# Kernel optimization log

Hardware: AMD Instinct MI355X
Metric: run time of the kernel (lower is better)

Reference implementation:

```python
import jax, jax.numpy as jnp
import numpy as np

B, C, L = 8, 512, 2048
HEADS, DIM_HEAD = 8, 64
HID = HEADS * DIM_HEAD  # 512


def setup_inputs() -> dict:
    key = jax.random.key(0)
    k1, k2, k3, k4 = jax.random.split(key, 4)
    x = jax.random.normal(k1, (B, C, L), dtype=jnp.float32)
    # Conv1d kernel_size=1 weights stored as [out, in] matrices
    w_qkv = jax.random.normal(k2, (3 * HID, C), dtype=jnp.float32) * (1.0 / np.sqrt(C))
    w_out = jax.random.normal(k3, (C, HID), dtype=jnp.float32) * (1.0 / np.sqrt(HID))
    b_out = jax.random.normal(k4, (C,), dtype=jnp.float32) * 0.01
    return {"x": x, "w_qkv": w_qkv, "w_out": w_out, "b_out": b_out}


def reference(x, w_qkv, w_out, b_out):
    scale = DIM_HEAD ** (-0.5)
    # 1x1 conv == channel-wise linear: [b,c,l] -> [b,3*hid,l]
    qkv = jnp.einsum('oc,bcl->bol', w_qkv, x)
    q, k, v = jnp.split(qkv, 3, axis=1)
    # split heads: b (h d) l -> b h d l
    split = lambda t: t.reshape(x.shape[0], HEADS, DIM_HEAD, t.shape[-1])
    q, k, v = split(q) * scale, split(k), split(v)
    sim = jnp.einsum('bhdi,bhdj->bhij', q, k)  # [b,h,l,l]
    attn = jax.nn.softmax(sim, axis=-1)
    out = jnp.einsum('bhij,bhdj->bhid', attn, v)  # [b,h,l,d]
    # b h l d -> b (h d) l
    out = jnp.transpose(out, (0, 1, 3, 2)).reshape(x.shape[0], HID, x.shape[-1])
    return jnp.einsum('oc,bcl->bol', w_out, out) + b_out[None, :, None]
```

## Files before the change

kernel.cpp:

```cpp
#include <hip/hip_runtime.h>

#define NB 8
#define NC 512
#define NL 2048
#define NH 8
#define ND 64
#define NHID 512

typedef float f32x4 __attribute__((ext_vector_type(4)));
typedef short bf16x8 __attribute__((ext_vector_type(8)));
typedef unsigned uint32x2 __attribute__((ext_vector_type(2)));
typedef unsigned uint32x4 __attribute__((ext_vector_type(4)));

__device__ __forceinline__ unsigned short f2bf(float x) {
    unsigned u = __float_as_uint(x);
    u += 0x7fffu + ((u >> 16) & 1u);
    return (unsigned short)(u >> 16);
}

__device__ __forceinline__ unsigned pack_bf16_ru(float lo, float hi) {
    unsigned a = __float_as_uint(lo) + 0x8000u;
    unsigned b = __float_as_uint(hi) + 0x8000u;
#if __has_builtin(__builtin_amdgcn_perm)
    return __builtin_amdgcn_perm(b, a, 0x07060302u);
#else
    return (a >> 16) | (b & 0xffff0000u);
#endif
}

__device__ __forceinline__ float fexp2(float x) {
#if __has_builtin(__builtin_amdgcn_exp2f)
    return __builtin_amdgcn_exp2f(x);
#else
    return exp2f(x);
#endif
}

__device__ __forceinline__ void gll16(const unsigned short* g, unsigned short* l) {
    __builtin_amdgcn_global_load_lds(
        (const __attribute__((address_space(1))) unsigned int*)g,
        (__attribute__((address_space(3))) unsigned int*)l, 16, 0, 0);
}

__device__ __forceinline__ void pfr_quad_swap(unsigned &a, unsigned &b) {
#if __has_builtin(__builtin_amdgcn_permlane32_swap) && __has_builtin(__builtin_amdgcn_permlane16_swap)
    uint32x2 r0 = __builtin_amdgcn_permlane32_swap(a, b, false, false);
    uint32x2 r1 = __builtin_amdgcn_permlane16_swap(r0[0], r0[1], false, false);
    a = r1[0];
    b = r1[1];
#else
    const int lane = (int)(threadIdx.x & 63);
    const int li = lane & 15, quad = lane >> 4;
    const int s0 = (li + ((quad & 1) << 5)) << 2;
    const int s1 = (li + 16 + ((quad & 1) << 5)) << 2;
    int ra = __builtin_amdgcn_ds_bpermute(s0, (int)a);
    int rb = __builtin_amdgcn_ds_bpermute(s0, (int)b);
    int ta = __builtin_amdgcn_ds_bpermute(s1, (int)a);
    int tb = __builtin_amdgcn_ds_bpermute(s1, (int)b);
    const bool lo = quad < 2;
    a = (unsigned)(lo ? ra : rb);
    b = (unsigned)(lo ? ta : tb);
#endif
}

__global__ __launch_bounds__(256) void xpose_kernel(
    const float* __restrict__ x, unsigned short* __restrict__ xT)
{
    __shared__ unsigned short T[64 * 65];
    const int tid = threadIdx.x;
    const int l0 = blockIdx.x * 64, c0 = blockIdx.y * 64, b = blockIdx.z;

    const int ll = tid & 63, cl0 = tid >> 6;
    #pragma unroll
    for (int i = 0; i < 16; i++) {
        const int cl = cl0 + 4 * i;
        T[cl * 65 + ll] = f2bf(x[((size_t)(b * NC + c0 + cl)) * NL + l0 + ll]);
    }
    __syncthreads();
    const int cg = tid & 7, lr = tid >> 3;
    #pragma unroll
    for (int rep = 0; rep < 2; rep++) {
        const int l = lr + rep * 32;
        unsigned u[4];
        #pragma unroll
        for (int j = 0; j < 4; j++) {
            unsigned short a = T[(cg * 8 + 2 * j) * 65 + l];
            unsigned short c = T[(cg * 8 + 2 * j + 1) * 65 + l];
            u[j] = (unsigned)a | ((unsigned)c << 16);
        }
        uint4 val; val.x = u[0]; val.y = u[1]; val.z = u[2]; val.w = u[3];
        *(uint4*)&xT[((size_t)(b * NL + l0 + l)) * NC + c0 + cg * 8] = val;
    }
}

__global__ __launch_bounds__(256) void wconv_kernel(
    const float* __restrict__ src, unsigned short* __restrict__ dst,
    int n8, int nscale8, float scale)
{
    const int idx = blockIdx.x * 256 + threadIdx.x;
    if (idx >= n8) return;
    const float s = (idx < nscale8) ? scale : 1.0f;
    float4 a = *(const float4*)&src[(size_t)idx * 8];
    float4 c = *(const float4*)&src[(size_t)idx * 8 + 4];
    uint4 val;
    val.x = (unsigned)f2bf(a.x * s) | ((unsigned)f2bf(a.y * s) << 16);
    val.y = (unsigned)f2bf(a.z * s) | ((unsigned)f2bf(a.w * s) << 16);
    val.z = (unsigned)f2bf(c.x * s) | ((unsigned)f2bf(c.y * s) << 16);
    val.w = (unsigned)f2bf(c.z * s) | ((unsigned)f2bf(c.w * s) << 16);
    *(uint4*)&dst[(size_t)idx * 8] = val;
}

__global__ __launch_bounds__(256) void qkv_proj_kernel(
    const unsigned short* __restrict__ xT, const unsigned short* __restrict__ wq,
    unsigned short* __restrict__ qb, unsigned short* __restrict__ kb,
    unsigned short* __restrict__ vb)
{
    __shared__ __align__(16) unsigned short Xt[128 * 64];
    __shared__ __align__(16) unsigned short Wt[128 * 64];
    const int tid = threadIdx.x;
    const int wave = tid >> 6, lane = tid & 63;
    const int quad = lane >> 4, li = lane & 15;
    const int o0 = blockIdx.x * 128, l0 = blockIdx.y * 128, b = blockIdx.z;

    const f32x4 fzero = {0.f, 0.f, 0.f, 0.f};
    f32x4 acc[2][8];
    #pragma unroll
    for (int mt = 0; mt < 2; mt++)
        #pragma unroll
        for (int nt = 0; nt < 8; nt++) acc[mt][nt] = fzero;

    const int srow = lane >> 3, schk = lane & 7;

    for (int c0 = 0; c0 < NC; c0 += 64) {
        #pragma unroll
        for (int i = 0; i < 4; i++) {
            const int r = wave * 32 + i * 8 + srow;
            gll16(xT + ((size_t)(b * NL + l0 + r)) * NC + c0 + ((schk ^ (r & 7)) * 8),
                  &Xt[(wave * 32 + i * 8) * 64]);
            gll16(wq + (size_t)(o0 + r) * NC + c0 + ((schk ^ (r & 7)) * 8),
                  &Wt[(wave * 32 + i * 8) * 64]);
        }
        __syncthreads();
        #pragma unroll
        for (int kc = 0; kc < 2; kc++) {
            const int sw = ((kc * 4 + quad) ^ (li & 7)) * 8;
            bf16x8 afr0 = *(const bf16x8*)&Xt[(wave * 32 + li) * 64 + sw];
            bf16x8 afr1 = *(const bf16x8*)&Xt[(wave * 32 + 16 + li) * 64 + sw];
            #pragma unroll
            for (int nt = 0; nt < 8; nt++) {
                bf16x8 bfr = *(const bf16x8*)&Wt[(nt * 16 + li) * 64 + sw];
                acc[0][nt] = __builtin_amdgcn_mfma_f32_16x16x32_bf16(afr0, bfr, acc[0][nt], 0, 0, 0);
                acc[1][nt] = __builtin_amdgcn_mfma_f32_16x16x32_bf16(afr1, bfr, acc[1][nt], 0, 0, 0);
            }
        }
        __syncthreads();
    }

    const int lr0 = l0 + wave * 32;
    if (o0 < 1024) {
        unsigned short* dst = (o0 < 512) ? qb : kb;
        #pragma unroll
        for (int mt = 0; mt < 2; mt++)
            #pragma unroll
            for (int nt = 0; nt < 8; nt++) {
                int oc = (o0 & 511) + nt * 16 + li;
                int hh = oc >> 6, d = oc & 63;
                size_t base =
                    ((size_t)((b * NH + hh) * NL) + lr0 + mt * 16 + quad * 4) * ND + d;
                #pragma unroll
                for (int r = 0; r < 4; r++)
                    dst[base + (size_t)r * ND] = f2bf(acc[mt][nt][r]);
            }
    } else {
        #pragma unroll
        for (int mt = 0; mt < 2; mt++)
            #pragma unroll
            for (int nt = 0; nt < 8; nt++) {
                int oc = (o0 - 1024) + nt * 16 + li;
                int hh = oc >> 6, d = oc & 63;
                size_t base = ((size_t)((b * NH + hh) * ND) + d) * NL +
                              lr0 + mt * 16 + quad * 4;
                uint2 pv;
                pv.x = (unsigned)f2bf(acc[mt][nt][0]) | ((unsigned)f2bf(acc[mt][nt][1]) << 16);
                pv.y = (unsigned)f2bf(acc[mt][nt][2]) | ((unsigned)f2bf(acc[mt][nt][3]) << 16);
                *(uint2*)&vb[base] = pv;
            }
    }
}

__global__ __launch_bounds__(256, 4) void attn_kernel(
    const unsigned short* __restrict__ qb, const unsigned short* __restrict__ kb,
    const unsigned short* __restrict__ vb, unsigned short* __restrict__ at)
{
    __shared__ __align__(16) unsigned short Kt[2][64 * 64];
    __shared__ __align__(16) unsigned short Vt[2][64 * 64];
    const int tid = threadIdx.x;
    const int wave = tid >> 6, lane = tid & 63;
    const int quad = lane >> 4, li = lane & 15;
    const int qt = blockIdx.x, h = blockIdx.y, b = blockIdx.z;
    const int bh = b * NH + h;
    const unsigned short* Qb = qb + (size_t)bh * NL * ND;
    const unsigned short* Kb = kb + (size_t)bh * NL * ND;
    const unsigned short* Vb = vb + (size_t)bh * ND * NL;

    bf16x8 qfr[2][2];
    #pragma unroll
    for (int mt = 0; mt < 2; mt++)
        #pragma unroll
        for (int kc = 0; kc < 2; kc++)
            qfr[mt][kc] = *(const bf16x8*)&Qb[(size_t)(qt * 128 + wave * 32 + mt * 16 + li) * ND +
                                             kc * 32 + quad * 8];

    const f32x4 fzero = {0.f, 0.f, 0.f, 0.f};
    f32x4 oacc[2][4];
    #pragma unroll
    for (int mt = 0; mt < 2; mt++)
        #pragma unroll
        for (int dt = 0; dt < 4; dt++) oacc[mt][dt] = fzero;

    f32x4 lsacc0 = fzero, lsacc1 = fzero;
    const short one_bf = (short)0x3F80;
    const bf16x8 ones = {one_bf, one_bf, one_bf, one_bf,
                         one_bf, one_bf, one_bf, one_bf};

    const int rrow = lane >> 3;
    const int rchk = lane & 7;

    auto stage = [&](int buf, int j0) {
        #pragma unroll
        for (int i = 0; i < 2; i++) {
            const int jrow = wave * 16 + i * 8 + rrow;
            gll16(Kb + (size_t)(j0 + jrow) * ND + ((rchk ^ (jrow & 7)) * 8),
                  &Kt[buf][(wave * 16 + i * 8) * 64]);
            const int drow = wave * 16 + i * 8 + rrow;
            gll16(Vb + (size_t)drow * NL + j0 + ((rchk ^ (drow & 7)) * 8),
                  &Vt[buf][(wave * 16 + i * 8) * 64]);
        }
    };

    stage(0, 0);
    __syncthreads();

    #pragma unroll 2
    for (int kt = 0; kt < 32; kt++) {
        const int cur = kt & 1;
        if (kt < 31) stage(cur ^ 1, (kt + 1) * 64);

        #pragma unroll
        for (int c = 0; c < 2; c++) {
            f32x4 st00 = fzero, st01 = fzero, st10 = fzero, st11 = fzero;
            #pragma unroll
            for (int dk = 0; dk < 2; dk++) {
                const int sw = ((dk * 4 + quad) ^ (li & 7)) * 8;
                bf16x8 kf0 = *(const bf16x8*)&Kt[cur][((2 * c + 0) * 16 + li) * 64 + sw];
                bf16x8 kf1 = *(const bf16x8*)&Kt[cur][((2 * c + 1) * 16 + li) * 64 + sw];
                st00 = __builtin_amdgcn_mfma_f32_16x16x32_bf16(kf0, qfr[0][dk], st00, 0, 0, 0);
                st01 = __builtin_amdgcn_mfma_f32_16x16x32_bf16(kf1, qfr[0][dk], st01, 0, 0, 0);
                st10 = __builtin_amdgcn_mfma_f32_16x16x32_bf16(kf0, qfr[1][dk], st10, 0, 0, 0);
                st11 = __builtin_amdgcn_mfma_f32_16x16x32_bf16(kf1, qfr[1][dk], st11, 0, 0, 0);
            }

            unsigned p000, p001, p010, p011, p100, p101, p110, p111;
            {
                float a0 = fexp2(st00[0]), a1 = fexp2(st00[1]),
                      a2 = fexp2(st00[2]), a3 = fexp2(st00[3]);
                float b0 = fexp2(st01[0]), b1 = fexp2(st01[1]),
                      b2 = fexp2(st01[2]), b3 = fexp2(st01[3]);
                p000 = pack_bf16_ru(a0, a1); p001 = pack_bf16_ru(a2, a3);
                p010 = pack_bf16_ru(b0, b1); p011 = pack_bf16_ru(b2, b3);
            }
            {
                float a0 = fexp2(st10[0]), a1 = fexp2(st10[1]),
                      a2 = fexp2(st10[2]), a3 = fexp2(st10[3]);
                float b0 = fexp2(st11[0]), b1 = fexp2(st11[1]),
                      b2 = fexp2(st11[2]), b3 = fexp2(st11[3]);
                p100 = pack_bf16_ru(a0, a1); p101 = pack_bf16_ru(a2, a3);
                p110 = pack_bf16_ru(b0, b1); p111 = pack_bf16_ru(b2, b3);
            }

            pfr_quad_swap(p000, p010);
            pfr_quad_swap(p001, p011);
            pfr_quad_swap(p100, p110);
            pfr_quad_swap(p101, p111);

            uint32x4 u0 = {p000, p001, p010, p011};
            uint32x4 u1 = {p100, p101, p110, p111};
            bf16x8 pf0 = __builtin_bit_cast(bf16x8, u0);
            bf16x8 pf1 = __builtin_bit_cast(bf16x8, u1);

            lsacc0 = __builtin_amdgcn_mfma_f32_16x16x32_bf16(ones, pf0, lsacc0, 0, 0, 0);
            lsacc1 = __builtin_amdgcn_mfma_f32_16x16x32_bf16(ones, pf1, lsacc1, 0, 0, 0);

            #pragma unroll
            for (int dt = 0; dt < 4; dt++) {
                const int swv = ((c * 4 + quad) ^ (li & 7)) * 8;
                bf16x8 vfr = *(const bf16x8*)&Vt[cur][(dt * 16 + li) * 64 + swv];
                oacc[0][dt] = __builtin_amdgcn_mfma_f32_16x16x32_bf16(vfr, pf0, oacc[0][dt], 0, 0, 0);
                oacc[1][dt] = __builtin_amdgcn_mfma_f32_16x16x32_bf16(vfr, pf1, oacc[1][dt], 0, 0, 0);
            }
        }
        __syncthreads();
    }

    #pragma unroll
    for (int mt = 0; mt < 2; mt++) {
        const float rl = 1.0f / (mt ? lsacc1[0] : lsacc0[0]);
        const int l = qt * 128 + wave * 32 + mt * 16 + li;
        #pragma unroll
        for (int dt = 0; dt < 4; dt++) {
            uint2 ov;
            ov.x = (unsigned)f2bf(oacc[mt][dt][0] * rl) |
                   ((unsigned)f2bf(oacc[mt][dt][1] * rl) << 16);
            ov.y = (unsigned)f2bf(oacc[mt][dt][2] * rl) |
                   ((unsigned)f2bf(oacc[mt][dt][3] * rl) << 16);
            *(uint2*)&at[((size_t)(b * NL + l)) * NHID + h * ND + dt * 16 + quad * 4] = ov;
        }
    }
}

__global__ __launch_bounds__(256) void out_proj_kernel(
    const unsigned short* __restrict__ at, const unsigned short* __restrict__ wo,
    const float* __restrict__ bias, float* __restrict__ out)
{
    __shared__ __align__(16) unsigned short Wt[128 * 64];
    __shared__ __align__(16) unsigned short At[128 * 64];
    const int tid = threadIdx.x;
    const int wave = tid >> 6, lane = tid & 63;
    const int quad = lane >> 4, li = lane & 15;
    const int o0 = blockIdx.x * 128, l0 = blockIdx.y * 128, b = blockIdx.z;

    const f32x4 fzero = {0.f, 0.f, 0.f, 0.f};
    f32x4 acc[2][8];
    #pragma unroll
    for (int mt = 0; mt < 2; mt++)
        #pragma unroll
        for (int nt = 0; nt < 8; nt++) acc[mt][nt] = fzero;

    const int srow = lane >> 3, schk = lane & 7;

    for (int c0 = 0; c0 < NHID; c0 += 64) {
        #pragma unroll
        for (int i = 0; i < 4; i++) {
            const int r = wave * 32 + i * 8 + srow;
            gll16(wo + (size_t)(o0 + r) * NHID + c0 + ((schk ^ (r & 7)) * 8),
                  &Wt[(wave * 32 + i * 8) * 64]);
            gll16(at + ((size_t)(b * NL + l0 + r)) * NHID + c0 + ((schk ^ (r & 7)) * 8),
                  &At[(wave * 32 + i * 8) * 64]);
        }
        __syncthreads();
        #pragma unroll
        for (int kc = 0; kc < 2; kc++) {
            const int sw = ((kc * 4 + quad) ^ (li & 7)) * 8;
            bf16x8 afr0 = *(const bf16x8*)&Wt[(wave * 32 + li) * 64 + sw];
            bf16x8 afr1 = *(const bf16x8*)&Wt[(wave * 32 + 16 + li) * 64 + sw];
            #pragma unroll
            for (int nt = 0; nt < 8; nt++) {
                bf16x8 bfr = *(const bf16x8*)&At[(nt * 16 + li) * 64 + sw];
                acc[0][nt] = __builtin_amdgcn_mfma_f32_16x16x32_bf16(afr0, bfr, acc[0][nt], 0, 0, 0);
                acc[1][nt] = __builtin_amdgcn_mfma_f32_16x16x32_bf16(afr1, bfr, acc[1][nt], 0, 0, 0);
            }
        }
        __syncthreads();
    }

    #pragma unroll
    for (int mt = 0; mt < 2; mt++) {
        int or0 = o0 + wave * 32 + mt * 16 + quad * 4;
        #pragma unroll
        for (int nt = 0; nt < 8; nt++) {
            int l = l0 + nt * 16 + li;
            #pragma unroll
            for (int r = 0; r < 4; r++)
                out[((size_t)(b * NC + or0 + r)) * NL + l] = acc[mt][nt][r] + bias[or0 + r];
        }
    }
}

extern "C" void kernel_launch(void* const* d_in, const int* in_sizes, int n_in,
                              void* d_out, int out_size, void* d_ws, size_t ws_size,
                              hipStream_t stream) {
    const float* x = (const float*)d_in[0];
    const float* w_qkv = (const float*)d_in[1];
    const float* w_out = (const float*)d_in[2];
    const float* b_out = (const float*)d_in[3];
    float* out = (float*)d_out;

    unsigned short* ws = (unsigned short*)d_ws;
    const size_t SZ = (size_t)NB * NH * NL * ND;
    unsigned short* qb = ws;
    unsigned short* kb = qb + SZ;
    unsigned short* vb = kb + SZ;
    unsigned short* at = vb + SZ;
    unsigned short* xT = at + SZ;
    unsigned short* wqb = xT + SZ;
    unsigned short* wob = wqb + (size_t)3 * NHID * NC;

    xpose_kernel<<<dim3(NL / 64, NC / 64, NB), dim3(256), 0, stream>>>(x, xT);
    wconv_kernel<<<dim3((3 * NHID * NC / 8 + 255) / 256), dim3(256), 0, stream>>>(
        w_qkv, wqb, 3 * NHID * NC / 8, NHID * NC / 8, 0.125f * 1.44269504088896f);
    wconv_kernel<<<dim3((NC * NHID / 8 + 255) / 256), dim3(256), 0, stream>>>(
        w_out, wob, NC * NHID / 8, 0, 1.0f);

    qkv_proj_kernel<<<dim3(12, 16, 8), dim3(256), 0, stream>>>(xT, wqb, qb, kb, vb);
    attn_kernel<<<dim3(16, 8, 8), dim3(256), 0, stream>>>(qb, kb, vb, at);
    out_proj_kernel<<<dim3(4, 16, 8), dim3(256), 0, stream>>>(at, wob, b_out, out);
}
```

Before: 231.2 us.

## Split attention query tile across 8 waves of 16 rows each

The attention kernel now runs 512 threads per block, each wave owning 16 query rows instead of 32. The K/V tile staging is spread across 8 waves, so each wave loads half as much. This is meant to raise wave-level parallelism and occupancy and to cut register pressure per wave. In exchange each K and V fragment read from LDS is reused by only one query sub-tile rather than two, so LDS read traffic per MFMA roughly doubles.

```diff
diff --git a/kernel.cpp b/kernel.cpp
--- a/kernel.cpp
+++ b/kernel.cpp
@@ -188,7 +188,7 @@
     }
 }
 
-__global__ __launch_bounds__(256, 4) void attn_kernel(
+__global__ __launch_bounds__(512, 8) void attn_kernel(
     const unsigned short* __restrict__ qb, const unsigned short* __restrict__ kb,
     const unsigned short* __restrict__ vb, unsigned short* __restrict__ at)
 {
@@ -203,22 +203,18 @@
     const unsigned short* Kb = kb + (size_t)bh * NL * ND;
     const unsigned short* Vb = vb + (size_t)bh * ND * NL;
 
-    bf16x8 qfr[2][2];
-    #pragma unroll
-    for (int mt = 0; mt < 2; mt++)
-        #pragma unroll
-        for (int kc = 0; kc < 2; kc++)
-            qfr[mt][kc] = *(const bf16x8*)&Qb[(size_t)(qt * 128 + wave * 32 + mt * 16 + li) * ND +
-                                             kc * 32 + quad * 8];
+    bf16x8 qfr[2];
+    #pragma unroll
+    for (int kc = 0; kc < 2; kc++)
+        qfr[kc] = *(const bf16x8*)&Qb[(size_t)(qt * 128 + wave * 16 + li) * ND +
+                                      kc * 32 + quad * 8];
 
     const f32x4 fzero = {0.f, 0.f, 0.f, 0.f};
-    f32x4 oacc[2][4];
-    #pragma unroll
-    for (int mt = 0; mt < 2; mt++)
-        #pragma unroll
-        for (int dt = 0; dt < 4; dt++) oacc[mt][dt] = fzero;
-
-    f32x4 lsacc0 = fzero, lsacc1 = fzero;
+    f32x4 oacc[4];
+    #pragma unroll
+    for (int dt = 0; dt < 4; dt++) oacc[dt] = fzero;
+
+    f32x4 lsacc = fzero;
     const short one_bf = (short)0x3F80;
     const bf16x8 ones = {one_bf, one_bf, one_bf, one_bf,
                          one_bf, one_bf, one_bf, one_bf};
@@ -227,15 +223,12 @@
     const int rchk = lane & 7;
 
     auto stage = [&](int buf, int j0) {
-        #pragma unroll
-        for (int i = 0; i < 2; i++) {
-            const int jrow = wave * 16 + i * 8 + rrow;
-            gll16(Kb + (size_t)(j0 + jrow) * ND + ((rchk ^ (jrow & 7)) * 8),
-                  &Kt[buf][(wave * 16 + i * 8) * 64]);
-            const int drow = wave * 16 + i * 8 + rrow;
-            gll16(Vb + (size_t)drow * NL + j0 + ((rchk ^ (drow & 7)) * 8),
-                  &Vt[buf][(wave * 16 + i * 8) * 64]);
-        }
+        const int jrow = wave * 8 + rrow;
+        gll16(Kb + (size_t)(j0 + jrow) * ND + ((rchk ^ (jrow & 7)) * 8),
+              &Kt[buf][(wave * 8) * 64]);
+        const int drow = wave * 8 + rrow;
+        gll16(Vb + (size_t)drow * NL + j0 + ((rchk ^ (drow & 7)) * 8),
+              &Vt[buf][(wave * 8) * 64]);
     };
 
     stage(0, 0);
@@ -248,73 +241,54 @@
 
         #pragma unroll
         for (int c = 0; c < 2; c++) {
-            f32x4 st00 = fzero, st01 = fzero, st10 = fzero, st11 = fzero;
+            f32x4 st0 = fzero, st1 = fzero;
             #pragma unroll
             for (int dk = 0; dk < 2; dk++) {
                 const int sw = ((dk * 4 + quad) ^ (li & 7)) * 8;
                 bf16x8 kf0 = *(const bf16x8*)&Kt[cur][((2 * c + 0) * 16 + li) * 64 + sw];
                 bf16x8 kf1 = *(const bf16x8*)&Kt[cur][((2 * c + 1) * 16 + li) * 64 + sw];
-                st00 = __builtin_amdgcn_mfma_f32_16x16x32_bf16(kf0, qfr[0][dk], st00, 0, 0, 0);
-                st01 = __builtin_amdgcn_mfma_f32_16x16x32_bf16(kf1, qfr[0][dk], st01, 0, 0, 0);
-                st10 = __builtin_amdgcn_mfma_f32_16x16x32_bf16(kf0, qfr[1][dk], st10, 0, 0, 0);
-                st11 = __builtin_amdgcn_mfma_f32_16x16x32_bf16(kf1, qfr[1][dk], st11, 0, 0, 0);
-            }
-
-            unsigned p000, p001, p010, p011, p100, p101, p110, p111;
+                st0 = __builtin_amdgcn_mfma_f32_16x16x32_bf16(kf0, qfr[dk], st0, 0, 0, 0);
+                st1 = __builtin_amdgcn_mfma_f32_16x16x32_bf16(kf1, qfr[dk], st1, 0, 0, 0);
+            }
+
+            unsigned p00, p01, p10, p11;
             {
-                float a0 = fexp2(st00[0]), a1 = fexp2(st00[1]),
-                      a2 = fexp2(st00[2]), a3 = fexp2(st00[3]);
-                float b0 = fexp2(st01[0]), b1 = fexp2(st01[1]),
-                      b2 = fexp2(st01[2]), b3 = fexp2(st01[3]);
-                p000 = pack_bf16_ru(a0, a1); p001 = pack_bf16_ru(a2, a3);
-                p010 = pack_bf16_ru(b0, b1); p011 = pack_bf16_ru(b2, b3);
-            }
-            {
-                float a0 = fexp2(st10[0]), a1 = fexp2(st10[1]),
-                      a2 = fexp2(st10[2]), a3 = fexp2(st10[3]);
-                float b0 = fexp2(st11[0]), b1 = fexp2(st11[1]),
-                      b2 = fexp2(st11[2]), b3 = fexp2(st11[3]);
-                p100 = pack_bf16_ru(a0, a1); p101 = pack_bf16_ru(a2, a3);
-                p110 = pack_bf16_ru(b0, b1); p111 = pack_bf16_ru(b2, b3);
-            }
-
-            pfr_quad_swap(p000, p010);
-            pfr_quad_swap(p001, p011);
-            pfr_quad_swap(p100, p110);
-            pfr_quad_swap(p101, p111);
-
-            uint32x4 u0 = {p000, p001, p010, p011};
-            uint32x4 u1 = {p100, p101, p110, p111};
-            bf16x8 pf0 = __builtin_bit_cast(bf16x8, u0);
-            bf16x8 pf1 = __builtin_bit_cast(bf16x8, u1);
-
-            lsacc0 = __builtin_amdgcn_mfma_f32_16x16x32_bf16(ones, pf0, lsacc0, 0, 0, 0);
-            lsacc1 = __builtin_amdgcn_mfma_f32_16x16x32_bf16(ones, pf1, lsacc1, 0, 0, 0);
+                float a0 = fexp2(st0[0]), a1 = fexp2(st0[1]),
+                      a2 = fexp2(st0[2]), a3 = fexp2(st0[3]);
+                float b0 = fexp2(st1[0]), b1 = fexp2(st1[1]),
+                      b2 = fexp2(st1[2]), b3 = fexp2(st1[3]);
+                p00 = pack_bf16_ru(a0, a1); p01 = pack_bf16_ru(a2, a3);
+                p10 = pack_bf16_ru(b0, b1); p11 = pack_bf16_ru(b2, b3);
+            }
+
+            pfr_quad_swap(p00, p10);
+            pfr_quad_swap(p01, p11);
+
+            uint32x4 u0 = {p00, p01, p10, p11};
+            bf16x8 pf = __builtin_bit_cast(bf16x8, u0);
+
+            lsacc = __builtin_amdgcn_mfma_f32_16x16x32_bf16(ones, pf, lsacc, 0, 0, 0);
 
             #pragma unroll
             for (int dt = 0; dt < 4; dt++) {
                 const int swv = ((c * 4 + quad) ^ (li & 7)) * 8;
                 bf16x8 vfr = *(const bf16x8*)&Vt[cur][(dt * 16 + li) * 64 + swv];
-                oacc[0][dt] = __builtin_amdgcn_mfma_f32_16x16x32_bf16(vfr, pf0, oacc[0][dt], 0, 0, 0);
-                oacc[1][dt] = __builtin_amdgcn_mfma_f32_16x16x32_bf16(vfr, pf1, oacc[1][dt], 0, 0, 0);
-            }
-        }
-        __syncthreads();
-    }
-
-    #pragma unroll
-    for (int mt = 0; mt < 2; mt++) {
-        const float rl = 1.0f / (mt ? lsacc1[0] : lsacc0[0]);
-        const int l = qt * 128 + wave * 32 + mt * 16 + li;
-        #pragma unroll
-        for (int dt = 0; dt < 4; dt++) {
-            uint2 ov;
-            ov.x = (unsigned)f2bf(oacc[mt][dt][0] * rl) |
-                   ((unsigned)f2bf(oacc[mt][dt][1] * rl) << 16);
-            ov.y = (unsigned)f2bf(oacc[mt][dt][2] * rl) |
-                   ((unsigned)f2bf(oacc[mt][dt][3] * rl) << 16);
-            *(uint2*)&at[((size_t)(b * NL + l)) * NHID + h * ND + dt * 16 + quad * 4] = ov;
-        }
+                oacc[dt] = __builtin_amdgcn_mfma_f32_16x16x32_bf16(vfr, pf, oacc[dt], 0, 0, 0);
+            }
+        }
+        __syncthreads();
+    }
+
+    const float rl = 1.0f / lsacc[0];
+    const int l = qt * 128 + wave * 16 + li;
+    #pragma unroll
+    for (int dt = 0; dt < 4; dt++) {
+        uint2 ov;
+        ov.x = (unsigned)f2bf(oacc[dt][0] * rl) |
+               ((unsigned)f2bf(oacc[dt][1] * rl) << 16);
+        ov.y = (unsigned)f2bf(oacc[dt][2] * rl) |
+               ((unsigned)f2bf(oacc[dt][3] * rl) << 16);
+        *(uint2*)&at[((size_t)(b * NL + l)) * NHID + h * ND + dt * 16 + quad * 4] = ov;
     }
 }
 
@@ -402,6 +376,6 @@
         w_out, wob, NC * NHID / 8, 0, 1.0f);
 
     qkv_proj_kernel<<<dim3(12, 16, 8), dim3(256), 0, stream>>>(xT, wqb, qb, kb, vb);
-    attn_kernel<<<dim3(16, 8, 8), dim3(256), 0, stream>>>(qb, kb, vb, at);
+    attn_kernel<<<dim3(16, 8, 8), dim3(512), 0, stream>>>(qb, kb, vb, at);
     out_proj_kernel<<<dim3(4, 16, 8), dim3(256), 0, stream>>>(at, wob, b_out, out);
 }
```

Measured after the change: 241.5 us. 1.04x slower.
